# Kernel optimization log

Hardware: AMD Instinct MI355X
Metric: run time of the kernel (lower is better)

Reference implementation:

```python
import jax, jax.numpy as jnp
import numpy as np

B, D = 4096, 256
TEMP = 0.5
EPS = 1e-8  # torch CosineSimilarity eps


def setup_inputs() -> dict:
    key = jax.random.key(0)
    k1, k2 = jax.random.split(key)
    return {
        "proj1": jax.random.normal(k1, (B, D), dtype=jnp.float32),
        "proj2": jax.random.normal(k2, (B, D), dtype=jnp.float32),
    }


def reference(proj1, proj2):
    b = proj1.shape[0]
    n = 2 * b
    z = jnp.concatenate([proj1, proj2], axis=0)  # [2B, D]
    # cosine similarity with clamped norms (matches torch.nn.CosineSimilarity)
    norm = jnp.maximum(jnp.linalg.norm(z, axis=1, keepdims=True), EPS)
    zn = z / norm
    sim = (zn @ zn.T) / TEMP  # [2B, 2B]
    # positives: diag(sim, +B) and diag(sim, -B)
    pos = jnp.concatenate([jnp.diagonal(sim, b), jnp.diagonal(sim, -b)])  # [2B]
    # CE with label 0 over logits [pos, negatives]. The negatives exclude the
    # diagonal and the positive pair, but the positive is re-included as
    # logits[:, 0], so the logsumexp runs over all entries except the diagonal.
    diag_mask = jnp.eye(n, dtype=bool)
    lse = jax.nn.logsumexp(jnp.where(diag_mask, -jnp.inf, sim), axis=1)  # [2B]
    loss = jnp.sum(lse - pos) / n
    return loss
```

## Files before the change

kernel.cpp:

```cpp
#include <hip/hip_runtime.h>
#include <hip/hip_bf16.h>

#define N_TOT 8192
#define B_HALF 4096
#define D_DIM 256
#define NQUAD 496
#define NSING 96
#define NBLK (NQUAD + NSING)
#define NREP 8

typedef __attribute__((ext_vector_type(4))) float f32x4;
typedef unsigned long long u64;

#define S8SCALE 27.178307f
#define LN2 0.69314718056f

__global__ __launch_bounds__(256) void k_norm(const float* __restrict__ p1,
                                              const float* __restrict__ p2,
                                              u64* __restrict__ zt,
                                              float* __restrict__ self,
                                              float* __restrict__ partials,
                                              float* __restrict__ RS,
                                              float* __restrict__ out) {
  __shared__ unsigned sm[2][8][64];
  __shared__ float red[4];
  int tid = threadIdx.x;
  int lane = tid & 63;
  int w = tid >> 6;
  int bid = blockIdx.x;
  int i0 = bid * 8;
  if (tid < 32) reinterpret_cast<f32x4*>(RS)[bid * 32 + tid] = (f32x4){0.f, 0.f, 0.f, 0.f};
  if (bid == 0 && tid == 0) out[0] = 0.0f;

  float possum = 0.f;
#pragma unroll
  for (int k = 0; k < 2; ++k) {
    int r = w * 2 + k;
    int i = i0 + r;
    float4 a = *reinterpret_cast<const float4*>(p1 + (size_t)i * D_DIM + lane * 4);
    float4 b = *reinterpret_cast<const float4*>(p2 + (size_t)i * D_DIM + lane * 4);
    float ssa = a.x * a.x + a.y * a.y + a.z * a.z + a.w * a.w;
    float ssb = b.x * b.x + b.y * b.y + b.z * b.z + b.w * b.w;
    float d = a.x * b.x + a.y * b.y + a.z * b.z + a.w * b.w;
#pragma unroll
    for (int m = 1; m < 64; m <<= 1) {
      ssa += __shfl_xor(ssa, m, 64);
      ssb += __shfl_xor(ssb, m, 64);
      d += __shfl_xor(d, m, 64);
    }
    float na = fmaxf(sqrtf(ssa), 1e-8f);
    float nb = fmaxf(sqrtf(ssb), 1e-8f);
    float ia = S8SCALE / na, ib = S8SCALE / nb;

    int wa = __builtin_amdgcn_cvt_pk_fp8_f32(a.x * ia, a.y * ia, 0, false);
    wa = __builtin_amdgcn_cvt_pk_fp8_f32(a.z * ia, a.w * ia, wa, true);
    int wb = __builtin_amdgcn_cvt_pk_fp8_f32(b.x * ib, b.y * ib, 0, false);
    wb = __builtin_amdgcn_cvt_pk_fp8_f32(b.z * ib, b.w * ib, wb, true);
    sm[0][r][lane] = (unsigned)wa;
    sm[1][r][lane] = (unsigned)wb;

    float va0 = __builtin_amdgcn_cvt_f32_fp8(wa, 0);
    float va1 = __builtin_amdgcn_cvt_f32_fp8(wa, 1);
    float va2 = __builtin_amdgcn_cvt_f32_fp8(wa, 2);
    float va3 = __builtin_amdgcn_cvt_f32_fp8(wa, 3);
    float vb0 = __builtin_amdgcn_cvt_f32_fp8(wb, 0);
    float vb1 = __builtin_amdgcn_cvt_f32_fp8(wb, 1);
    float vb2 = __builtin_amdgcn_cvt_f32_fp8(wb, 2);
    float vb3 = __builtin_amdgcn_cvt_f32_fp8(wb, 3);
    float sqa = va0 * va0 + va1 * va1 + va2 * va2 + va3 * va3;
    float sqb = vb0 * vb0 + vb1 * vb1 + vb2 * vb2 + vb3 * vb3;
#pragma unroll
    for (int m = 1; m < 64; m <<= 1) {
      sqa += __shfl_xor(sqa, m, 64);
      sqb += __shfl_xor(sqb, m, 64);
    }
    if (lane == 0) {
      self[i] = sqa * (1.0f / 256.0f);
      self[i + B_HALF] = sqb * (1.0f / 256.0f);
      possum += -4.0f * d / (na * nb) * (1.0f / (float)N_TOT);
    }
  }
  if (lane == 0) red[w] = possum;
  __syncthreads();
  if (tid == 0) partials[bid] = red[0] + red[1] + red[2] + red[3];

  {
    int h = tid >> 7;
    int rem = tid & 127;
    int g = rem >> 2;
    int qr = rem & 3;
    uint4 v;
    v.x = sm[h][qr * 2][g * 2];
    v.y = sm[h][qr * 2][g * 2 + 1];
    v.z = sm[h][qr * 2 + 1][g * 2];
    v.w = sm[h][qr * 2 + 1][g * 2 + 1];
    size_t idx8 = (size_t)g * N_TOT + h * B_HALF + i0 + qr * 2;
    *reinterpret_cast<uint4*>((char*)zt + idx8 * 8) = v;
  }
}

__global__ __launch_bounds__(256, 3) void k_sim(const u64* __restrict__ zt,
                                                float* __restrict__ RS) {
  const int bid = blockIdx.x;
  int ti = 0, cum = 0, tj0, nt;
  if (bid < NQUAD) {
    while (cum + ((64 - ti) >> 2) <= bid) { cum += (64 - ti) >> 2; ++ti; }
    tj0 = ti + 4 * (bid - cum);
    nt = 4;
  } else {
    const int s = bid - NQUAD;
    while (cum + ((64 - ti) & 3) <= s) { cum += (64 - ti) & 3; ++ti; }
    tj0 = 64 - ((64 - ti) & 3) + (s - cum);
    nt = 1;
  }
  const int nht = 2 * nt;
  const bool diag = (tj0 == ti);
  const int rowbase = ti * 128;
  const int colchunk = tj0 * 128;
  float* __restrict__ rowsum = RS + (size_t)(bid & (NREP - 1)) * N_TOT;

  const int tid = threadIdx.x;
  const int lane = tid & 63;
  const int wid = tid >> 6;
  const int wm = wid >> 1;
  const int wn = wid & 1;
  const int hi = lane >> 4;
  const int lo = lane & 15;

  const size_t baseA = (size_t)hi * N_TOT + rowbase + wm * 64 + lo;
  const size_t baseB = (size_t)hi * N_TOT + colchunk + wn * 32 + lo;

  long af[4][8];
#pragma unroll
  for (int m = 0; m < 4; ++m)
#pragma unroll
    for (int g = 0; g < 8; ++g)
      af[m][g] = (long)zt[(size_t)g * 4 * N_TOT + baseA + m * 16];

  float pr[4][4] = {};

  long bf[2][8];
#pragma unroll 1
  for (int t = 0; t < nht; ++t) {
#pragma unroll
    for (int n = 0; n < 2; ++n)
#pragma unroll
      for (int g = 0; g < 8; ++g)
        bf[n][g] = (long)zt[(size_t)g * 4 * N_TOT + baseB + t * 64 + n * 16];

    f32x4 acc[4][2];
#pragma unroll
    for (int m = 0; m < 4; ++m)
#pragma unroll
      for (int n = 0; n < 2; ++n) acc[m][n] = (f32x4){0.f, 0.f, 0.f, 0.f};
#pragma unroll
    for (int g = 0; g < 8; ++g)
#pragma unroll
      for (int m = 0; m < 4; ++m) {
        acc[m][0] = __builtin_amdgcn_mfma_f32_16x16x32_fp8_fp8(
            af[m][g], bf[0][g], acc[m][0], 0, 0, 0);
        acc[m][1] = __builtin_amdgcn_mfma_f32_16x16x32_fp8_fp8(
            af[m][g], bf[1][g], acc[m][1], 0, 0, 0);
      }

    float pc[2] = {0.f, 0.f};
#pragma unroll
    for (int m = 0; m < 4; ++m)
#pragma unroll
      for (int n = 0; n < 2; ++n) {
        float e0 = __builtin_amdgcn_exp2f(acc[m][n][0] * (1.0f / 256.0f));
        float e1 = __builtin_amdgcn_exp2f(acc[m][n][1] * (1.0f / 256.0f));
        float e2 = __builtin_amdgcn_exp2f(acc[m][n][2] * (1.0f / 256.0f));
        float e3 = __builtin_amdgcn_exp2f(acc[m][n][3] * (1.0f / 256.0f));
        pr[m][0] += e0; pr[m][1] += e1; pr[m][2] += e2; pr[m][3] += e3;
        pc[n] += (e0 + e1) + (e2 + e3);
      }

    if (!(diag && t < 2)) {
#pragma unroll
      for (int n = 0; n < 2; ++n) {
        float v = pc[n];
        v += __shfl_xor(v, 16, 64);
        v += __shfl_xor(v, 32, 64);
        if (hi == 0)
          atomicAdd(&rowsum[colchunk + t * 64 + wn * 32 + n * 16 + lo], v);
      }
    }
  }

#pragma unroll
  for (int m = 0; m < 4; ++m)
#pragma unroll
    for (int r = 0; r < 4; ++r) {
      float s = pr[m][r];
      s += __shfl_xor(s, 1, 64);
      s += __shfl_xor(s, 2, 64);
      s += __shfl_xor(s, 4, 64);
      s += __shfl_xor(s, 8, 64);
      if (lo == 0)
        atomicAdd(&rowsum[rowbase + wm * 64 + m * 16 + hi * 4 + r], s);
    }
}

__global__ __launch_bounds__(256) void k_lse(const float* __restrict__ RS,
                                             const float* __restrict__ self,
                                             const float* __restrict__ partials,
                                             float* __restrict__ out) {
  int tid = threadIdx.x;
  int i = blockIdx.x * 256 + tid;
  float rs = 0.f;
#pragma unroll
  for (int r = 0; r < NREP; ++r) rs += RS[(size_t)r * N_TOT + i];
  rs -= __builtin_amdgcn_exp2f(self[i]);
  float v = __builtin_amdgcn_logf(rs) * (LN2 / (float)N_TOT);
  if (tid < 16) v += partials[blockIdx.x * 16 + tid];
#pragma unroll
  for (int m = 1; m < 64; m <<= 1) v += __shfl_xor(v, m, 64);
  __shared__ float red[4];
  if ((tid & 63) == 0) red[tid >> 6] = v;
  __syncthreads();
  if (tid == 0) atomicAdd(out, red[0] + red[1] + red[2] + red[3]);
}

extern "C" void kernel_launch(void* const* d_in, const int* in_sizes, int n_in,
                              void* d_out, int out_size, void* d_ws, size_t ws_size,
                              hipStream_t stream) {
  const float* p1 = (const float*)d_in[0];
  const float* p2 = (const float*)d_in[1];
  float* out = (float*)d_out;
  char* ws = (char*)d_ws;

  u64* zt = (u64*)ws;
  float* self = (float*)(ws + 2097152);
  float* RS = self + N_TOT;
  float* partials = RS + (size_t)NREP * N_TOT;

  k_norm<<<N_TOT / 16, 256, 0, stream>>>(p1, p2, zt, self, partials, RS, out);
  k_sim<<<NBLK, 256, 0, stream>>>(zt, RS);
  k_lse<<<N_TOT / 256, 256, 0, stream>>>(RS, self, partials, out);
}
```

Baseline: 36.09 us.

## Switch similarity tiles to 32x32x16 fp8 MFMA with 64-column warp subtiles

Replaces the 16x16x32 fp8 MFMA tiling with 32x32x16 fp8 MFMA. Each wave now computes a 64x64 subtile per iteration instead of 64x32, so the loop runs nt times instead of 2*nt. The fragment layouts, the row-sum and column-sum reductions and the atomic index mapping are rewritten to match the 32x32 accumulator layout. Launch bounds drop from 3 to 1 blocks per CU, which lets the compiler use more registers for the larger A and B fragments (32 longs each) but may reduce occupancy and latency hiding.

```diff
diff --git a/kernel.cpp b/kernel.cpp
--- a/kernel.cpp
+++ b/kernel.cpp
@@ -10,6 +10,7 @@
 #define NREP 8
 
 typedef __attribute__((ext_vector_type(4))) float f32x4;
+typedef __attribute__((ext_vector_type(16))) float f32x16;
 typedef unsigned long long u64;
 
 #define S8SCALE 27.178307f
@@ -99,7 +100,7 @@
   }
 }
 
-__global__ __launch_bounds__(256, 3) void k_sim(const u64* __restrict__ zt,
+__global__ __launch_bounds__(256, 1) void k_sim(const u64* __restrict__ zt,
                                                 float* __restrict__ RS) {
   const int bid = blockIdx.x;
   int ti = 0, cum = 0, tj0, nt;
@@ -113,7 +114,6 @@
     tj0 = 64 - ((64 - ti) & 3) + (s - cum);
     nt = 1;
   }
-  const int nht = 2 * nt;
   const bool diag = (tj0 == ti);
   const int rowbase = ti * 128;
   const int colchunk = tj0 * 128;
@@ -124,81 +124,80 @@
   const int wid = tid >> 6;
   const int wm = wid >> 1;
   const int wn = wid & 1;
-  const int hi = lane >> 4;
-  const int lo = lane & 15;
-
-  const size_t baseA = (size_t)hi * N_TOT + rowbase + wm * 64 + lo;
-  const size_t baseB = (size_t)hi * N_TOT + colchunk + wn * 32 + lo;
-
-  long af[4][8];
-#pragma unroll
-  for (int m = 0; m < 4; ++m)
-#pragma unroll
-    for (int g = 0; g < 8; ++g)
-      af[m][g] = (long)zt[(size_t)g * 4 * N_TOT + baseA + m * 16];
-
-  float pr[4][4] = {};
-
-  long bf[2][8];
+  const int c31 = lane & 31;
+  const int h5 = lane >> 5;
+
+  const size_t rowA = (size_t)(rowbase + wm * 64 + c31);
+  long af[2][16];
+#pragma unroll
+  for (int mb = 0; mb < 2; ++mb)
+#pragma unroll
+    for (int kk = 0; kk < 16; ++kk)
+      af[mb][kk] = (long)zt[(size_t)(2 * kk + h5) * N_TOT + rowA + mb * 32];
+
+  float pr[2][16] = {};
+
 #pragma unroll 1
-  for (int t = 0; t < nht; ++t) {
-#pragma unroll
-    for (int n = 0; n < 2; ++n)
-#pragma unroll
-      for (int g = 0; g < 8; ++g)
-        bf[n][g] = (long)zt[(size_t)g * 4 * N_TOT + baseB + t * 64 + n * 16];
-
-    f32x4 acc[4][2];
-#pragma unroll
-    for (int m = 0; m < 4; ++m)
-#pragma unroll
-      for (int n = 0; n < 2; ++n) acc[m][n] = (f32x4){0.f, 0.f, 0.f, 0.f};
-#pragma unroll
-    for (int g = 0; g < 8; ++g)
-#pragma unroll
-      for (int m = 0; m < 4; ++m) {
-        acc[m][0] = __builtin_amdgcn_mfma_f32_16x16x32_fp8_fp8(
-            af[m][g], bf[0][g], acc[m][0], 0, 0, 0);
-        acc[m][1] = __builtin_amdgcn_mfma_f32_16x16x32_fp8_fp8(
-            af[m][g], bf[1][g], acc[m][1], 0, 0, 0);
+  for (int t = 0; t < nt; ++t) {
+    const int colT = colchunk + t * 128 + wn * 64;
+    const size_t colB = (size_t)(colT + c31);
+
+    long bf[2][16];
+#pragma unroll
+    for (int nb = 0; nb < 2; ++nb)
+#pragma unroll
+      for (int kk = 0; kk < 16; ++kk)
+        bf[nb][kk] = (long)zt[(size_t)(2 * kk + h5) * N_TOT + colB + nb * 32];
+
+    f32x16 acc[2][2];
+#pragma unroll
+    for (int mb = 0; mb < 2; ++mb)
+#pragma unroll
+      for (int nb = 0; nb < 2; ++nb)
+#pragma unroll
+        for (int r = 0; r < 16; ++r) acc[mb][nb][r] = 0.f;
+
+#pragma unroll
+    for (int kk = 0; kk < 16; ++kk) {
+      acc[0][0] = __builtin_amdgcn_mfma_f32_32x32x16_fp8_fp8(af[0][kk], bf[0][kk], acc[0][0], 0, 0, 0);
+      acc[0][1] = __builtin_amdgcn_mfma_f32_32x32x16_fp8_fp8(af[0][kk], bf[1][kk], acc[0][1], 0, 0, 0);
+      acc[1][0] = __builtin_amdgcn_mfma_f32_32x32x16_fp8_fp8(af[1][kk], bf[0][kk], acc[1][0], 0, 0, 0);
+      acc[1][1] = __builtin_amdgcn_mfma_f32_32x32x16_fp8_fp8(af[1][kk], bf[1][kk], acc[1][1], 0, 0, 0);
+    }
+
+#pragma unroll
+    for (int nb = 0; nb < 2; ++nb) {
+      float pc = 0.f;
+#pragma unroll
+      for (int mb = 0; mb < 2; ++mb)
+#pragma unroll
+        for (int r = 0; r < 16; ++r) {
+          float e = __builtin_amdgcn_exp2f(acc[mb][nb][r] * (1.0f / 256.0f));
+          pr[mb][r] += e;
+          pc += e;
+        }
+      if (!(diag && t == 0)) {
+        float v = pc + __shfl_xor(pc, 32, 64);
+        if (h5 == 0)
+          atomicAdd(&rowsum[colT + nb * 32 + c31], v);
       }
-
-    float pc[2] = {0.f, 0.f};
-#pragma unroll
-    for (int m = 0; m < 4; ++m)
-#pragma unroll
-      for (int n = 0; n < 2; ++n) {
-        float e0 = __builtin_amdgcn_exp2f(acc[m][n][0] * (1.0f / 256.0f));
-        float e1 = __builtin_amdgcn_exp2f(acc[m][n][1] * (1.0f / 256.0f));
-        float e2 = __builtin_amdgcn_exp2f(acc[m][n][2] * (1.0f / 256.0f));
-        float e3 = __builtin_amdgcn_exp2f(acc[m][n][3] * (1.0f / 256.0f));
-        pr[m][0] += e0; pr[m][1] += e1; pr[m][2] += e2; pr[m][3] += e3;
-        pc[n] += (e0 + e1) + (e2 + e3);
-      }
-
-    if (!(diag && t < 2)) {
-#pragma unroll
-      for (int n = 0; n < 2; ++n) {
-        float v = pc[n];
-        v += __shfl_xor(v, 16, 64);
-        v += __shfl_xor(v, 32, 64);
-        if (hi == 0)
-          atomicAdd(&rowsum[colchunk + t * 64 + wn * 32 + n * 16 + lo], v);
-      }
-    }
-  }
-
-#pragma unroll
-  for (int m = 0; m < 4; ++m)
-#pragma unroll
-    for (int r = 0; r < 4; ++r) {
-      float s = pr[m][r];
+    }
+  }
+
+#pragma unroll
+  for (int mb = 0; mb < 2; ++mb)
+#pragma unroll
+    for (int r = 0; r < 16; ++r) {
+      float s = pr[mb][r];
       s += __shfl_xor(s, 1, 64);
       s += __shfl_xor(s, 2, 64);
       s += __shfl_xor(s, 4, 64);
       s += __shfl_xor(s, 8, 64);
-      if (lo == 0)
-        atomicAdd(&rowsum[rowbase + wm * 64 + m * 16 + hi * 4 + r], s);
+      s += __shfl_xor(s, 16, 64);
+      if (c31 == 0) {
+        int row = rowbase + wm * 64 + mb * 32 + (r & 3) + 8 * (r >> 2) + 4 * h5;
+        atomicAdd(&rowsum[row], s);
+      }
     }
 }
 
```

New measurement: 54.57 us. +51.2%, slower.

## Split row tile across four waves with 32x32 sub-tiles and raise occupancy

Applied to the files above, without the earlier changes.

Each wave now owns 32 rows of the 128-row block and sweeps all columns in 32-wide steps, replacing the 2x2 wave grid with 64x64 per-wave tiles. This halves the A fragment registers and accumulators so the launch bound can request 4 blocks per SIMD instead of 3. In exchange each wave reloads B fragments more often from global memory, and more column atomics are issued because every wave covers every column step.

```diff
diff --git a/kernel.cpp b/kernel.cpp
--- a/kernel.cpp
+++ b/kernel.cpp
@@ -99,7 +99,7 @@
   }
 }
 
-__global__ __launch_bounds__(256, 3) void k_sim(const u64* __restrict__ zt,
+__global__ __launch_bounds__(256, 4) void k_sim(const u64* __restrict__ zt,
                                                 float* __restrict__ RS) {
   const int bid = blockIdx.x;
   int ti = 0, cum = 0, tj0, nt;
@@ -113,7 +113,7 @@
     tj0 = 64 - ((64 - ti) & 3) + (s - cum);
     nt = 1;
   }
-  const int nht = 2 * nt;
+  const int nht = 4 * nt;
   const bool diag = (tj0 == ti);
   const int rowbase = ti * 128;
   const int colchunk = tj0 * 128;
@@ -122,83 +122,80 @@
   const int tid = threadIdx.x;
   const int lane = tid & 63;
   const int wid = tid >> 6;
-  const int wm = wid >> 1;
-  const int wn = wid & 1;
   const int hi = lane >> 4;
   const int lo = lane & 15;
 
-  const size_t baseA = (size_t)hi * N_TOT + rowbase + wm * 64 + lo;
-  const size_t baseB = (size_t)hi * N_TOT + colchunk + wn * 32 + lo;
-
-  long af[4][8];
-#pragma unroll
-  for (int m = 0; m < 4; ++m)
+  const size_t baseA = (size_t)hi * N_TOT + rowbase + wid * 32 + lo;
+
+  long af[2][8];
+#pragma unroll
+  for (int mb = 0; mb < 2; ++mb)
 #pragma unroll
     for (int g = 0; g < 8; ++g)
-      af[m][g] = (long)zt[(size_t)g * 4 * N_TOT + baseA + m * 16];
-
-  float pr[4][4] = {};
+      af[mb][g] = (long)zt[(size_t)g * 4 * N_TOT + baseA + mb * 16];
+
+  float pr[2][4] = {};
 
   long bf[2][8];
 #pragma unroll 1
   for (int t = 0; t < nht; ++t) {
-#pragma unroll
-    for (int n = 0; n < 2; ++n)
+    const int colT = colchunk + t * 32;
+    const size_t baseB = (size_t)hi * N_TOT + colT + lo;
+#pragma unroll
+    for (int nb = 0; nb < 2; ++nb)
 #pragma unroll
       for (int g = 0; g < 8; ++g)
-        bf[n][g] = (long)zt[(size_t)g * 4 * N_TOT + baseB + t * 64 + n * 16];
-
-    f32x4 acc[4][2];
-#pragma unroll
-    for (int m = 0; m < 4; ++m)
-#pragma unroll
-      for (int n = 0; n < 2; ++n) acc[m][n] = (f32x4){0.f, 0.f, 0.f, 0.f};
-#pragma unroll
-    for (int g = 0; g < 8; ++g)
-#pragma unroll
-      for (int m = 0; m < 4; ++m) {
-        acc[m][0] = __builtin_amdgcn_mfma_f32_16x16x32_fp8_fp8(
-            af[m][g], bf[0][g], acc[m][0], 0, 0, 0);
-        acc[m][1] = __builtin_amdgcn_mfma_f32_16x16x32_fp8_fp8(
-            af[m][g], bf[1][g], acc[m][1], 0, 0, 0);
+        bf[nb][g] = (long)zt[(size_t)g * 4 * N_TOT + baseB + nb * 16];
+
+    f32x4 acc[2][2];
+#pragma unroll
+    for (int mb = 0; mb < 2; ++mb)
+#pragma unroll
+      for (int nb = 0; nb < 2; ++nb) acc[mb][nb] = (f32x4){0.f, 0.f, 0.f, 0.f};
+#pragma unroll
+    for (int g = 0; g < 8; ++g) {
+      acc[0][0] = __builtin_amdgcn_mfma_f32_16x16x32_fp8_fp8(af[0][g], bf[0][g], acc[0][0], 0, 0, 0);
+      acc[0][1] = __builtin_amdgcn_mfma_f32_16x16x32_fp8_fp8(af[0][g], bf[1][g], acc[0][1], 0, 0, 0);
+      acc[1][0] = __builtin_amdgcn_mfma_f32_16x16x32_fp8_fp8(af[1][g], bf[0][g], acc[1][0], 0, 0, 0);
+      acc[1][1] = __builtin_amdgcn_mfma_f32_16x16x32_fp8_fp8(af[1][g], bf[1][g], acc[1][1], 0, 0, 0);
+    }
+
+    float pc[2] = {0.f, 0.f};
+#pragma unroll
+    for (int mb = 0; mb < 2; ++mb)
+#pragma unroll
+      for (int nb = 0; nb < 2; ++nb) {
+        float e0 = __builtin_amdgcn_exp2f(acc[mb][nb][0] * (1.0f / 256.0f));
+        float e1 = __builtin_amdgcn_exp2f(acc[mb][nb][1] * (1.0f / 256.0f));
+        float e2 = __builtin_amdgcn_exp2f(acc[mb][nb][2] * (1.0f / 256.0f));
+        float e3 = __builtin_amdgcn_exp2f(acc[mb][nb][3] * (1.0f / 256.0f));
+        pr[mb][0] += e0; pr[mb][1] += e1; pr[mb][2] += e2; pr[mb][3] += e3;
+        pc[nb] += (e0 + e1) + (e2 + e3);
       }
 
-    float pc[2] = {0.f, 0.f};
-#pragma unroll
-    for (int m = 0; m < 4; ++m)
-#pragma unroll
-      for (int n = 0; n < 2; ++n) {
-        float e0 = __builtin_amdgcn_exp2f(acc[m][n][0] * (1.0f / 256.0f));
-        float e1 = __builtin_amdgcn_exp2f(acc[m][n][1] * (1.0f / 256.0f));
-        float e2 = __builtin_amdgcn_exp2f(acc[m][n][2] * (1.0f / 256.0f));
-        float e3 = __builtin_amdgcn_exp2f(acc[m][n][3] * (1.0f / 256.0f));
-        pr[m][0] += e0; pr[m][1] += e1; pr[m][2] += e2; pr[m][3] += e3;
-        pc[n] += (e0 + e1) + (e2 + e3);
-      }
-
-    if (!(diag && t < 2)) {
-#pragma unroll
-      for (int n = 0; n < 2; ++n) {
-        float v = pc[n];
+    if (!(diag && t < 4)) {
+#pragma unroll
+      for (int nb = 0; nb < 2; ++nb) {
+        float v = pc[nb];
         v += __shfl_xor(v, 16, 64);
         v += __shfl_xor(v, 32, 64);
         if (hi == 0)
-          atomicAdd(&rowsum[colchunk + t * 64 + wn * 32 + n * 16 + lo], v);
+          atomicAdd(&rowsum[colT + nb * 16 + lo], v);
       }
     }
   }
 
 #pragma unroll
-  for (int m = 0; m < 4; ++m)
+  for (int mb = 0; mb < 2; ++mb)
 #pragma unroll
     for (int r = 0; r < 4; ++r) {
-      float s = pr[m][r];
+      float s = pr[mb][r];
       s += __shfl_xor(s, 1, 64);
       s += __shfl_xor(s, 2, 64);
       s += __shfl_xor(s, 4, 64);
       s += __shfl_xor(s, 8, 64);
       if (lo == 0)
-        atomicAdd(&rowsum[rowbase + wm * 64 + m * 16 + hi * 4 + r], s);
+        atomicAdd(&rowsum[rowbase + wid * 32 + mb * 16 + hi * 4 + r], s);
     }
 }
 
```

Result: slower. 42.37 us (+17.4%).

## Defer column-sum atomics one iteration to overlap with B-fragment loads

Applied to the files above, without the earlier changes.

In the similarity kernel, the per-tile column-sum atomics are held back and issued in the next iteration, right after that iteration's B-fragment loads. An explicit `s_waitcnt vmcnt(2)`, fenced by scheduling barriers, lets the MFMAs start while those two atomics are still in flight. The aim is to hide the atomic latency and the load latency behind the matrix work. Launch bounds drop from 3 to 1 blocks per CU, which frees registers but may lower occupancy. Diagonal tiles now issue zero-valued atomics instead of skipping them, and the handwritten waitcnt depends on in-order vmcnt accounting.

```diff
diff --git a/kernel.cpp b/kernel.cpp
--- a/kernel.cpp
+++ b/kernel.cpp
@@ -99,7 +99,7 @@
   }
 }
 
-__global__ __launch_bounds__(256, 3) void k_sim(const u64* __restrict__ zt,
+__global__ __launch_bounds__(256, 1) void k_sim(const u64* __restrict__ zt,
                                                 float* __restrict__ RS) {
   const int bid = blockIdx.x;
   int ti = 0, cum = 0, tj0, nt;
@@ -138,15 +138,30 @@
       af[m][g] = (long)zt[(size_t)g * 4 * N_TOT + baseA + m * 16];
 
   float pr[4][4] = {};
-
   long bf[2][8];
+  float fl0 = 0.f, fl1 = 0.f;
+  int colPrev = 0;
+
 #pragma unroll 1
   for (int t = 0; t < nht; ++t) {
-#pragma unroll
-    for (int n = 0; n < 2; ++n)
+    const int colT = colchunk + t * 64 + wn * 32;
+#pragma unroll
+    for (int nb = 0; nb < 2; ++nb)
 #pragma unroll
       for (int g = 0; g < 8; ++g)
-        bf[n][g] = (long)zt[(size_t)g * 4 * N_TOT + baseB + t * 64 + n * 16];
+        bf[nb][g] = (long)zt[(size_t)g * 4 * N_TOT + baseB + t * 64 + nb * 16];
+    __builtin_amdgcn_sched_barrier(0);
+    if (t > 0 && hi == 0) {
+      atomicAdd(&rowsum[colPrev + lo], fl0);
+      atomicAdd(&rowsum[colPrev + 16 + lo], fl1);
+    }
+    __builtin_amdgcn_sched_barrier(0);
+    if (t == 0) {
+      asm volatile("s_waitcnt vmcnt(0)" ::: "memory");
+    } else {
+      asm volatile("s_waitcnt vmcnt(2)" ::: "memory");
+    }
+    __builtin_amdgcn_sched_barrier(0);
 
     f32x4 acc[4][2];
 #pragma unroll
@@ -154,14 +169,16 @@
 #pragma unroll
       for (int n = 0; n < 2; ++n) acc[m][n] = (f32x4){0.f, 0.f, 0.f, 0.f};
 #pragma unroll
-    for (int g = 0; g < 8; ++g)
-#pragma unroll
-      for (int m = 0; m < 4; ++m) {
-        acc[m][0] = __builtin_amdgcn_mfma_f32_16x16x32_fp8_fp8(
-            af[m][g], bf[0][g], acc[m][0], 0, 0, 0);
-        acc[m][1] = __builtin_amdgcn_mfma_f32_16x16x32_fp8_fp8(
-            af[m][g], bf[1][g], acc[m][1], 0, 0, 0);
-      }
+    for (int g = 0; g < 8; ++g) {
+      acc[0][0] = __builtin_amdgcn_mfma_f32_16x16x32_fp8_fp8(af[0][g], bf[0][g], acc[0][0], 0, 0, 0);
+      acc[0][1] = __builtin_amdgcn_mfma_f32_16x16x32_fp8_fp8(af[0][g], bf[1][g], acc[0][1], 0, 0, 0);
+      acc[1][0] = __builtin_amdgcn_mfma_f32_16x16x32_fp8_fp8(af[1][g], bf[0][g], acc[1][0], 0, 0, 0);
+      acc[1][1] = __builtin_amdgcn_mfma_f32_16x16x32_fp8_fp8(af[1][g], bf[1][g], acc[1][1], 0, 0, 0);
+      acc[2][0] = __builtin_amdgcn_mfma_f32_16x16x32_fp8_fp8(af[2][g], bf[0][g], acc[2][0], 0, 0, 0);
+      acc[2][1] = __builtin_amdgcn_mfma_f32_16x16x32_fp8_fp8(af[2][g], bf[1][g], acc[2][1], 0, 0, 0);
+      acc[3][0] = __builtin_amdgcn_mfma_f32_16x16x32_fp8_fp8(af[3][g], bf[0][g], acc[3][0], 0, 0, 0);
+      acc[3][1] = __builtin_amdgcn_mfma_f32_16x16x32_fp8_fp8(af[3][g], bf[1][g], acc[3][1], 0, 0, 0);
+    }
 
     float pc[2] = {0.f, 0.f};
 #pragma unroll
@@ -175,17 +192,20 @@
         pr[m][0] += e0; pr[m][1] += e1; pr[m][2] += e2; pr[m][3] += e3;
         pc[n] += (e0 + e1) + (e2 + e3);
       }
-
-    if (!(diag && t < 2)) {
-#pragma unroll
-      for (int n = 0; n < 2; ++n) {
-        float v = pc[n];
-        v += __shfl_xor(v, 16, 64);
-        v += __shfl_xor(v, 32, 64);
-        if (hi == 0)
-          atomicAdd(&rowsum[colchunk + t * 64 + wn * 32 + n * 16 + lo], v);
-      }
-    }
+    float v0 = pc[0];
+    v0 += __shfl_xor(v0, 16, 64);
+    v0 += __shfl_xor(v0, 32, 64);
+    float v1 = pc[1];
+    v1 += __shfl_xor(v1, 16, 64);
+    v1 += __shfl_xor(v1, 32, 64);
+    const bool skip = (diag && t < 2);
+    fl0 = skip ? 0.f : v0;
+    fl1 = skip ? 0.f : v1;
+    colPrev = colT;
+  }
+  if (hi == 0) {
+    atomicAdd(&rowsum[colPrev + lo], fl0);
+    atomicAdd(&rowsum[colPrev + 16 + lo], fl1);
   }
 
 #pragma unroll
```

Measured after the change: 34.07 us. 1.06x faster.
